# Kernel optimization log

Measured on AMD Instinct MI355X. Metric: run time of the kernel, lower is better.

Reference implementation:

```python
import jax, jax.numpy as jnp
import numpy as np

B, T, V, E, H = 64, 64, 32000, 512, 1024


def setup_inputs() -> dict:
    key = jax.random.key(0)
    ks = jax.random.split(key, 12)
    s = 0.02
    return {
        "hidden": jax.random.normal(ks[0], (2, B, H), jnp.float32),
        "cell": jax.random.normal(ks[1], (2, B, H), jnp.float32),
        "captions": jax.random.randint(ks[2], (B, T), 0, V, jnp.int32),
        "embed_W": jax.random.normal(ks[3], (V, E), jnp.float32) * s,
        "W_ih0": jax.random.normal(ks[4], (4 * H, E), jnp.float32) * s,
        "W_hh0": jax.random.normal(ks[5], (4 * H, H), jnp.float32) * s,
        "b_ih0": jnp.zeros((4 * H,), jnp.float32),
        "b_hh0": jnp.zeros((4 * H,), jnp.float32),
        "W_ih1": jax.random.normal(ks[6], (4 * H, H), jnp.float32) * s,
        "W_hh1": jax.random.normal(ks[7], (4 * H, H), jnp.float32) * s,
        "b_ih1": jnp.zeros((4 * H,), jnp.float32),
        "b_hh1": jnp.zeros((4 * H,), jnp.float32),
        "Wp_voc": jax.random.normal(ks[8], (V, H), jnp.float32) * s,
        "bp_voc": jnp.zeros((V,), jnp.float32),
    }


def lstm_cell(x, h, c, W_ih, W_hh, b):
    # PyTorch gate order: input, forget, cell(g), output
    gates = x @ W_ih.T + h @ W_hh.T + b  # [B, 4H]
    i, f, g, o = jnp.split(gates, 4, axis=-1)
    i, f, o = jax.nn.sigmoid(i), jax.nn.sigmoid(f), jax.nn.sigmoid(o)
    g = jnp.tanh(g)
    c_new = f * c + i * g
    h_new = o * jnp.tanh(c_new)
    return h_new, c_new


def reference(hidden, cell, captions, embed_W, W_ih0, W_hh0, b_ih0, b_hh0,
              W_ih1, W_hh1, b_ih1, b_hh1, Wp_voc, bp_voc):
    # teacher forcing (ratio=1.0): LSTM input at step t is embed(captions[:, t-1])
    x_seq = embed_W[captions[:, :-1]]        # [B, T-1, E]
    x_seq = jnp.swapaxes(x_seq, 0, 1)        # [T-1, B, E] time-major for scan
    b0 = b_ih0 + b_hh0
    b1 = b_ih1 + b_hh1

    def step(carry, x):
        h0, c0, h1, c1 = carry
        h0, c0 = lstm_cell(x, h0, c0, W_ih0, W_hh0, b0)
        h1, c1 = lstm_cell(h0, h1, c1, W_ih1, W_hh1, b1)
        logits = h1 @ Wp_voc.T + bp_voc      # [B, V]
        return (h0, c0, h1, c1), logits

    carry = (hidden[0], cell[0], hidden[1], cell[1])
    _, logits = jax.lax.scan(step, carry, x_seq)   # [T-1, B, V]
    logits = jnp.swapaxes(logits, 0, 1)            # [B, T-1, V]
    # outputs[:, 0, :] stays zero as in the torch code
    return jnp.concatenate([jnp.zeros((logits.shape[0], 1, logits.shape[2]), logits.dtype), logits], axis=1)
```

## Files before the change

kernel.cpp:

```cpp
#include <hip/hip_runtime.h>

#define B_    64
#define T_    64
#define V_    32000
#define E_    512
#define H_    1024
#define G4_   4096
#define TS_   63
#define MROWS 4032
#define MPAD  4096
#define BH    (B_ * H_)
#define FPAD  32

typedef __attribute__((ext_vector_type(8))) short bf16x8;
typedef __attribute__((ext_vector_type(4))) float f32x4;
typedef __attribute__((ext_vector_type(4))) unsigned int uint32x4;

__device__ __forceinline__ unsigned short bfbits(float f) {
  union { float f; unsigned int u; } cv; cv.f = f;
  unsigned int u = cv.u;
  u += 0x7fffu + ((u >> 16) & 1u);
  return (unsigned short)(u >> 16);
}
__device__ __forceinline__ float bf2f(unsigned short h) {
  union { unsigned int u; float f; } cv; cv.u = ((unsigned int)h) << 16;
  return cv.f;
}
__device__ __forceinline__ float fsig(float x) { return 1.f / (1.f + __expf(-x)); }
__device__ __forceinline__ float ftanh(float x) {
  x = fminf(fmaxf(x, -10.f), 10.f);
  const float e = __expf(2.f * x);
  return (e - 1.f) / (e + 1.f);
}

__device__ __forceinline__ void store_dword_dc(void* p, unsigned int v) {
  asm volatile("global_store_dword %0, %1, off sc0 sc1" :: "v"(p), "v"(v) : "memory");
}
__device__ __forceinline__ void store_b128_dc(void* p, uint32x4 v) {
  asm volatile("global_store_dwordx4 %0, %1, off sc0 sc1" :: "v"(p), "v"(v) : "memory");
}
__device__ __forceinline__ unsigned int load_dword_dc(const void* p) {
  unsigned int v;
  asm volatile("global_load_dword %0, %1, off sc0 sc1\n\ts_waitcnt vmcnt(0)"
               : "=v"(v) : "v"(p) : "memory");
  return v;
}
__device__ __forceinline__ void store_dword_nt(void* p, float f) {
  union { float f; unsigned int u; } cv; cv.f = f;
  asm volatile("global_store_dword %0, %1, off nt" :: "v"(p), "v"(cv.u) : "memory");
}

__device__ __forceinline__ void gload16(const void* g, void* l) {
  __builtin_amdgcn_global_load_lds(
      (const __attribute__((address_space(1))) unsigned int*)g,
      (__attribute__((address_space(3))) unsigned int*)l, 16, 0, 0);
}


__global__ void k_cast4(const float4* __restrict__ s, ushort4* __restrict__ d, int n4) {
  int i = blockIdx.x * blockDim.x + threadIdx.x;
  const int st = gridDim.x * blockDim.x;
  for (; i < n4; i += st) {
    const float4 f = s[i];
    ushort4 v;
    v.x = bfbits(f.x); v.y = bfbits(f.y); v.z = bfbits(f.z); v.w = bfbits(f.w);
    d[i] = v;
  }
}

__global__ void k_bias(const float* __restrict__ a, const float* __restrict__ b,
                       float* __restrict__ o, int n) {
  const int i = blockIdx.x * blockDim.x + threadIdx.x;
  if (i < n) o[i] = a[i] + b[i];
}

__global__ void k_gather(const float* __restrict__ embed, const int* __restrict__ caps,
                         unsigned short* __restrict__ X) {
  const int i = blockIdx.x * 256 + threadIdx.x;
  const int m = i >> 7, e4 = i & 127;
  ushort4 v;
  if (m < MROWS) {
    const int t = m >> 6, b = m & 63;
    const int idx = caps[b * T_ + t];
    const float4 f = ((const float4*)embed)[(long)idx * (E_ / 4) + e4];
    v.x = bfbits(f.x); v.y = bfbits(f.y); v.z = bfbits(f.z); v.w = bfbits(f.w);
  } else {
    v = make_ushort4(0, 0, 0, 0);
  }
  ((ushort4*)X)[i] = v;
}

__global__ void k_init(const float* __restrict__ hidden, const float* __restrict__ cell,
                       unsigned short* __restrict__ H0, unsigned short* __restrict__ H1,
                       float* __restrict__ c0, float* __restrict__ c1,
                       unsigned int* __restrict__ flags) {
  const int i = blockIdx.x * 256 + threadIdx.x;
  H0[i] = bfbits(hidden[i]);
  H1[i] = bfbits(hidden[B_ * H_ + i]);
  c0[i] = cell[i];
  c1[i] = cell[B_ * H_ + i];
  if (i < 192 * FPAD) flags[i] = 0u;
}

__global__ void k_zeropad(unsigned short* __restrict__ a, unsigned short* __restrict__ b) {
  const int i = blockIdx.x * 256 + threadIdx.x;
  a[i] = 0;
  b[i] = 0;
}

__global__ void k_zero_t0(float4* __restrict__ out4) {
  const int i = blockIdx.x * 256 + threadIdx.x;
  const int b = i / (V_ / 4), v = i - b * (V_ / 4);
  out4[(long)b * (T_ * V_ / 4) + v] = make_float4(0.f, 0.f, 0.f, 0.f);
}

template <int KDIM, bool TO_OUT>
__global__ __launch_bounds__(256) void k_gemm(
    const unsigned short* __restrict__ A, const unsigned short* __restrict__ Bm,
    const float* __restrict__ bias, unsigned short* __restrict__ Cb,
    float* __restrict__ Cout, int N) {
  __shared__ unsigned short As[128 * 32];
  __shared__ unsigned short Bs[128 * 32];
  const int tid = threadIdx.x;
  const int w = tid >> 6, l = tid & 63;
  const int wm = (w >> 1) * 64, wn = (w & 1) * 64;
  const int lr = l & 15, lk = (l >> 4) * 8;
  const long am0 = (long)blockIdx.y * 128;
  const long bn0 = (long)blockIdx.x * 128;

  const int u0 = tid, u1 = tid + 256;
  const char* gA0 = (const char*)(A + (am0 + (u0 >> 2)) * KDIM) + (u0 & 3) * 16;
  const char* gA1 = (const char*)(A + (am0 + (u1 >> 2)) * KDIM) + (u1 & 3) * 16;
  const char* gB0 = (const char*)(Bm + (bn0 + (u0 >> 2)) * KDIM) + (u0 & 3) * 16;
  const char* gB1 = (const char*)(Bm + (bn0 + (u1 >> 2)) * KDIM) + (u1 & 3) * 16;
  char* lA0 = (char*)As + u0 * 16; char* lA1 = (char*)As + u1 * 16;
  char* lB0 = (char*)Bs + u0 * 16; char* lB1 = (char*)Bs + u1 * 16;

  f32x4 acc[4][4];
  const f32x4 z = {0.f, 0.f, 0.f, 0.f};
  #pragma unroll
  for (int mi = 0; mi < 4; ++mi)
    #pragma unroll
    for (int ni = 0; ni < 4; ++ni) acc[mi][ni] = z;

  for (int k0 = 0; k0 < KDIM; k0 += 32) {
    __syncthreads();
    gload16(gA0 + (long)k0 * 2, lA0);
    gload16(gA1 + (long)k0 * 2, lA1);
    gload16(gB0 + (long)k0 * 2, lB0);
    gload16(gB1 + (long)k0 * 2, lB1);
    __syncthreads();
    bf16x8 af[4], bfr[4];
    #pragma unroll
    for (int mi = 0; mi < 4; ++mi)
      af[mi] = *(const bf16x8*)(As + (wm + mi * 16 + lr) * 32 + lk);
    #pragma unroll
    for (int ni = 0; ni < 4; ++ni)
      bfr[ni] = *(const bf16x8*)(Bs + (wn + ni * 16 + lr) * 32 + lk);
    #pragma unroll
    for (int mi = 0; mi < 4; ++mi)
      #pragma unroll
      for (int ni = 0; ni < 4; ++ni)
        acc[mi][ni] = __builtin_amdgcn_mfma_f32_16x16x32_bf16(af[mi], bfr[ni], acc[mi][ni], 0, 0, 0);
  }

  #pragma unroll
  for (int ni = 0; ni < 4; ++ni) {
    const int n = (int)bn0 + wn + ni * 16 + lr;
    const float bv = bias[n];
    #pragma unroll
    for (int mi = 0; mi < 4; ++mi) {
      #pragma unroll
      for (int r = 0; r < 4; ++r) {
        const int m = (int)am0 + wm + mi * 16 + (l >> 4) * 4 + r;
        const float v = acc[mi][ni][r] + bv;
        if constexpr (TO_OUT) {
          if (m < MROWS) {
            const int t = m >> 6, b = m & 63;
            store_dword_nt(Cout + (long)(b * T_ + t + 1) * V_ + n, v);
          }
        } else {
          Cb[(long)m * N + n] = bfbits(v);
        }
      }
    }
  }
}

__global__ __launch_bounds__(256) void k_fused(
    const unsigned short* __restrict__ Whh0b,
    const unsigned short* __restrict__ Whh1b,
    const unsigned short* __restrict__ Wih1b,
    const unsigned short* __restrict__ Xp,
    unsigned short* __restrict__ H0b,
    unsigned short* __restrict__ H1b,
    const float* __restrict__ c0i, const float* __restrict__ c1i,
    const float* __restrict__ b1s,
    unsigned int* __restrict__ f0,
    unsigned int* __restrict__ f1) {
  __shared__ unsigned short Wl[64 * 1024];
  __shared__ __align__(16) float gs1[4][64][8];
  unsigned short (*hexch)[16] = (unsigned short (*)[16])gs1;

  const int tid = threadIdx.x;
  const int w = tid >> 6, l = tid & 63;
  const int lcol = l & 15, khi = l >> 4;
  const int bw = w * 16;
  const f32x4 z = {0.f, 0.f, 0.f, 0.f};

  if (blockIdx.x < 64) {
    const int blk = blockIdx.x;
    const int jb = blk << 4;
    for (int u = tid; u < 64 * 128; u += 256) {
      const int rr = u >> 7, cu = u & 127;
      const int g = rr >> 4, jj = rr & 15;
      ((bf16x8*)Wl)[rr * 128 + (cu ^ (rr & 7))] =
          *(const bf16x8*)(Whh0b + (size_t)(g * 1024 + jb + jj) * H_ + cu * 8);
    }
    f32x4 cr;
    #pragma unroll
    for (int r = 0; r < 4; ++r)
      cr[r] = c0i[(size_t)(bw + khi * 4 + r) * H_ + jb + lcol];
    unsigned short pin[16];
    #pragma unroll
    for (int r = 0; r < 4; ++r) {
      const unsigned short* ir = Xp + (size_t)(bw + khi * 4 + r) * G4_ + jb + lcol;
      pin[r * 4 + 0] = ir[0];
      pin[r * 4 + 1] = ir[H_];
      pin[r * 4 + 2] = ir[2 * H_];
      pin[r * 4 + 3] = ir[3 * H_];
    }
    __syncthreads();

    for (int s = 0; s < TS_; ++s) {
      if (s > 0) {
        if (tid < 64)
          while (load_dword_dc(&f0[tid << 5]) < (unsigned)s) {}
        __syncthreads();
      }
      f32x4 a0, a1, a2, a3;
      #pragma unroll
      for (int r = 0; r < 4; ++r) {
        a0[r] = bf2f(pin[r * 4 + 0]);
        a1[r] = bf2f(pin[r * 4 + 1]);
        a2[r] = bf2f(pin[r * 4 + 2]);
        a3[r] = bf2f(pin[r * 4 + 3]);
      }
      const unsigned short* hrow = H0b + (size_t)s * BH + (size_t)(bw + lcol) * H_ + khi * 8;
      #pragma unroll 8
      for (int kk = 0; kk < 32; ++kk) {
        const bf16x8 av = *(const bf16x8*)(hrow + kk * 32);
        const int un = (kk * 4 + khi) ^ (lcol & 7);
        const bf16x8 b0 = ((const bf16x8*)Wl)[(0 * 16 + lcol) * 128 + un];
        const bf16x8 b1 = ((const bf16x8*)Wl)[(1 * 16 + lcol) * 128 + un];
        const bf16x8 b2 = ((const bf16x8*)Wl)[(2 * 16 + lcol) * 128 + un];
        const bf16x8 b3 = ((const bf16x8*)Wl)[(3 * 16 + lcol) * 128 + un];
        a0 = __builtin_amdgcn_mfma_f32_16x16x32_bf16(av, b0, a0, 0, 0, 0);
        a1 = __builtin_amdgcn_mfma_f32_16x16x32_bf16(av, b1, a1, 0, 0, 0);
        a2 = __builtin_amdgcn_mfma_f32_16x16x32_bf16(av, b2, a2, 0, 0, 0);
        a3 = __builtin_amdgcn_mfma_f32_16x16x32_bf16(av, b3, a3, 0, 0, 0);
      }
      #pragma unroll
      for (int r = 0; r < 4; ++r) {
        const float gi = fsig(a0[r]);
        const float gf = fsig(a1[r]);
        const float gg = ftanh(a2[r]);
        const float go = fsig(a3[r]);
        cr[r] = gf * cr[r] + gi * gg;
        hexch[bw + khi * 4 + r][lcol] = bfbits(go * ftanh(cr[r]));
      }
      if (s + 1 < TS_) {
        const unsigned short* inb = Xp + (size_t)(s + 1) * (B_ * G4_);
        #pragma unroll
        for (int r = 0; r < 4; ++r) {
          const unsigned short* ir = inb + (size_t)(bw + khi * 4 + r) * G4_ + jb + lcol;
          pin[r * 4 + 0] = ir[0];
          pin[r * 4 + 1] = ir[H_];
          pin[r * 4 + 2] = ir[2 * H_];
          pin[r * 4 + 3] = ir[3 * H_];
        }
      }
      __syncthreads();
      if (tid < 128) {
        const int b = tid >> 1, hf = tid & 1;
        const uint32x4 v = *(const uint32x4*)&hexch[b][hf * 8];
        store_b128_dc(H0b + (size_t)(s + 1) * BH + (size_t)b * H_ + jb + hf * 8, v);
      }
      __syncthreads();
      if (tid == 0) store_dword_dc(&f0[blk << 5], (unsigned)(s + 1));
    }
  } else {
    const int blk1 = blockIdx.x - 64;
    const int jb1 = blk1 << 3;
    for (int u = tid; u < 64 * 128; u += 256) {
      const int pr = u >> 7, cu = u & 127;
      const int prl = pr & 31, tt = prl >> 4, lr_ = prl & 15;
      const int g = tt * 2 + (lr_ >> 3), jj = lr_ & 7;
      const unsigned short* src =
          ((pr >> 5) ? Wih1b : Whh1b) + (size_t)(g * 1024 + jb1 + jj) * H_ + cu * 8;
      ((bf16x8*)Wl)[pr * 128 + (cu ^ (pr & 7))] = *(const bf16x8*)src;
    }
    const int bb = tid >> 2;
    const int j0 = (tid * 2) & 7;
    float cA = c1i[(size_t)bb * H_ + jb1 + j0];
    float cB = c1i[(size_t)bb * H_ + jb1 + j0 + 1];
    float biA[4], biB[4];
    #pragma unroll
    for (int g = 0; g < 4; ++g) {
      biA[g] = b1s[g * 1024 + jb1 + j0];
      biB[g] = b1s[g * 1024 + jb1 + j0 + 1];
    }
    __syncthreads();

    for (int s = 1; s <= TS_; ++s) {
      {
        const unsigned t0 = (unsigned)s, t1 = (unsigned)(s - 1);
        if (tid < 64) {
          while (load_dword_dc(&f0[tid << 5]) < t0) {}
        } else if (tid < 192) {
          while (load_dword_dc(&f1[(tid - 64) << 5]) < t1) {}
        }
        __syncthreads();
      }
      f32x4 ac0 = z, ac1 = z;
      const unsigned short* a1p = H1b + (size_t)(s - 1) * BH + (size_t)(bw + lcol) * H_ + khi * 8;
      const unsigned short* a0p = H0b + (size_t)s * BH + (size_t)(bw + lcol) * H_ + khi * 8;
      #pragma unroll 8
      for (int kk = 0; kk < 32; ++kk) {
        const bf16x8 av = *(const bf16x8*)(a1p + kk * 32);
        const int un = (kk * 4 + khi) ^ (lcol & 7);
        const bf16x8 b0 = ((const bf16x8*)Wl)[(0 + lcol) * 128 + un];
        const bf16x8 b1 = ((const bf16x8*)Wl)[(16 + lcol) * 128 + un];
        ac0 = __builtin_amdgcn_mfma_f32_16x16x32_bf16(av, b0, ac0, 0, 0, 0);
        ac1 = __builtin_amdgcn_mfma_f32_16x16x32_bf16(av, b1, ac1, 0, 0, 0);
      }
      #pragma unroll 8
      for (int kk = 0; kk < 32; ++kk) {
        const bf16x8 av = *(const bf16x8*)(a0p + kk * 32);
        const int un = (kk * 4 + khi) ^ (lcol & 7);
        const bf16x8 b0 = ((const bf16x8*)Wl)[(32 + lcol) * 128 + un];
        const bf16x8 b1 = ((const bf16x8*)Wl)[(48 + lcol) * 128 + un];
        ac0 = __builtin_amdgcn_mfma_f32_16x16x32_bf16(av, b0, ac0, 0, 0, 0);
        ac1 = __builtin_amdgcn_mfma_f32_16x16x32_bf16(av, b1, ac1, 0, 0, 0);
      }
      #pragma unroll
      for (int r = 0; r < 4; ++r) {
        const int b = bw + khi * 4 + r;
        gs1[lcol >> 3][b][lcol & 7] = ac0[r];
        gs1[2 + (lcol >> 3)][b][lcol & 7] = ac1[r];
      }
      __syncthreads();
      {
        const float giA = fsig(gs1[0][bb][j0] + biA[0]);
        const float gfA = fsig(gs1[1][bb][j0] + biA[1]);
        const float ggA = ftanh(gs1[2][bb][j0] + biA[2]);
        const float goA = fsig(gs1[3][bb][j0] + biA[3]);
        cA = gfA * cA + giA * ggA;
        const unsigned short hA = bfbits(goA * ftanh(cA));
        const float giB = fsig(gs1[0][bb][j0 + 1] + biB[0]);
        const float gfB = fsig(gs1[1][bb][j0 + 1] + biB[1]);
        const float ggB = ftanh(gs1[2][bb][j0 + 1] + biB[2]);
        const float goB = fsig(gs1[3][bb][j0 + 1] + biB[3]);
        cB = gfB * cB + giB * ggB;
        const unsigned short hB = bfbits(goB * ftanh(cB));
        const unsigned int hv = ((unsigned int)hB << 16) | hA;
        store_dword_dc(H1b + (size_t)s * BH + (size_t)bb * H_ + jb1 + j0, hv);
      }
      __syncthreads();
      if (tid == 0) store_dword_dc(&f1[blk1 << 5], (unsigned)s);
    }
  }
}


extern "C" void kernel_launch(void* const* d_in, const int* in_sizes, int n_in,
                              void* d_out, int out_size, void* d_ws, size_t ws_size,
                              hipStream_t stream) {
  (void)in_sizes; (void)n_in; (void)out_size; (void)ws_size;
  const float* hidden = (const float*)d_in[0];
  const float* cell   = (const float*)d_in[1];
  const int*   caps   = (const int*)d_in[2];
  const float* embed  = (const float*)d_in[3];
  const float* Wih0   = (const float*)d_in[4];
  const float* Whh0   = (const float*)d_in[5];
  const float* bih0   = (const float*)d_in[6];
  const float* bhh0   = (const float*)d_in[7];
  const float* Wih1   = (const float*)d_in[8];
  const float* Whh1   = (const float*)d_in[9];
  const float* bih1   = (const float*)d_in[10];
  const float* bhh1   = (const float*)d_in[11];
  const float* Wp     = (const float*)d_in[12];
  const float* bp     = (const float*)d_in[13];
  float* out = (float*)d_out;

  char* p = (char*)d_ws;
  auto alloc = [&](size_t bytes) { char* r = p; p += (bytes + 255) & ~(size_t)255; return r; };
  unsigned short* Xbf   = (unsigned short*)alloc((size_t)MPAD * E_ * 2);
  unsigned short* Wih0b = (unsigned short*)alloc((size_t)G4_ * E_ * 2);
  unsigned short* Whh0b = (unsigned short*)alloc((size_t)G4_ * H_ * 2);
  unsigned short* Wih1b = (unsigned short*)alloc((size_t)G4_ * H_ * 2);
  unsigned short* Whh1b = (unsigned short*)alloc((size_t)G4_ * H_ * 2);
  unsigned short* Wpb   = (unsigned short*)alloc((size_t)V_ * H_ * 2);
  unsigned short* Xp    = (unsigned short*)alloc((size_t)MPAD * G4_ * 2);
  unsigned short* H0    = (unsigned short*)alloc((size_t)(MPAD + B_) * H_ * 2);
  unsigned short* H1    = (unsigned short*)alloc((size_t)(MPAD + B_) * H_ * 2);
  float* c0  = (float*)alloc((size_t)B_ * H_ * 4);
  float* c1  = (float*)alloc((size_t)B_ * H_ * 4);
  float* b0s = (float*)alloc((size_t)G4_ * 4);
  float* b1s = (float*)alloc((size_t)G4_ * 4);
  unsigned int* cbar = (unsigned int*)alloc((size_t)192 * FPAD * 4);

  k_cast4<<<2048, 256, 0, stream>>>((const float4*)Wih0, (ushort4*)Wih0b, G4_ * E_ / 4);
  k_cast4<<<2048, 256, 0, stream>>>((const float4*)Whh0, (ushort4*)Whh0b, G4_ * H_ / 4);
  k_cast4<<<2048, 256, 0, stream>>>((const float4*)Wih1, (ushort4*)Wih1b, G4_ * H_ / 4);
  k_cast4<<<2048, 256, 0, stream>>>((const float4*)Whh1, (ushort4*)Whh1b, G4_ * H_ / 4);
  k_cast4<<<4096, 256, 0, stream>>>((const float4*)Wp,   (ushort4*)Wpb,   V_ * H_ / 4);
  k_bias<<<16, 256, 0, stream>>>(bih0, bhh0, b0s, G4_);
  k_bias<<<16, 256, 0, stream>>>(bih1, bhh1, b1s, G4_);
  k_gather<<<2048, 256, 0, stream>>>(embed, caps, Xbf);
  k_init<<<256, 256, 0, stream>>>(hidden, cell, H0, H1, c0, c1, cbar);
  k_zeropad<<<256, 256, 0, stream>>>(H0 + (size_t)MPAD * H_, H1 + (size_t)MPAD * H_);
  k_zero_t0<<<2000, 256, 0, stream>>>((float4*)out);

  k_gemm<512, false><<<dim3(32, 32), 256, 0, stream>>>(Xbf, Wih0b, b0s, Xp, nullptr, G4_);

  k_fused<<<192, 256, 0, stream>>>(Whh0b, Whh1b, Wih1b, Xp, H0, H1, c0, c1, b1s,
                                   cbar, cbar + 64 * FPAD);

  k_gemm<1024, true><<<dim3(250, 32), 256, 0, stream>>>(H1 + (size_t)B_ * H_, Wpb, bp, nullptr, out, V_);
}
```

Measured before the change: 1.109 ms.

## Swizzle vocab GEMM block order for cache reuse and add sleep in spin-waits

The output projection GEMM now launches a flat 1D grid of 8192 blocks over a vocabulary dimension padded to 32768. Block indices are remapped so that consecutive blocks share the same N-columns of the weight tile across M rows, grouped into 8 chunks, to improve L2/MALL reuse of weight tiles. Bounds checks on n handle the padded region. Separately, the spin-wait loops in the fused LSTM kernel now call s_sleep to reduce memory polling pressure, which may add wake-up latency to every step. The padded weight rows past V are allocated but never initialised, so they hold garbage; their products are computed and then discarded, which wastes some work.

```diff
diff --git a/kernel.cpp b/kernel.cpp
--- a/kernel.cpp
+++ b/kernel.cpp
@@ -3,6 +3,7 @@
 #define B_    64
 #define T_    64
 #define V_    32000
+#define VPAD  32768
 #define E_    512
 #define H_    1024
 #define G4_   4096
@@ -114,7 +115,7 @@
   out4[(long)b * (T_ * V_ / 4) + v] = make_float4(0.f, 0.f, 0.f, 0.f);
 }
 
-template <int KDIM, bool TO_OUT>
+template <int KDIM, bool TO_OUT, bool SWZ>
 __global__ __launch_bounds__(256) void k_gemm(
     const unsigned short* __restrict__ A, const unsigned short* __restrict__ Bm,
     const float* __restrict__ bias, unsigned short* __restrict__ Cb,
@@ -125,8 +126,17 @@
   const int w = tid >> 6, l = tid & 63;
   const int wm = (w >> 1) * 64, wn = (w & 1) * 64;
   const int lr = l & 15, lk = (l >> 4) * 8;
-  const long am0 = (long)blockIdx.y * 128;
-  const long bn0 = (long)blockIdx.x * 128;
+  int bx, by;
+  if constexpr (SWZ) {
+    const int flat = blockIdx.x;
+    const int k = flat & 7, i = flat >> 3;
+    bx = (k << 5) + (i >> 5);
+    by = i & 31;
+  } else {
+    bx = blockIdx.x; by = blockIdx.y;
+  }
+  const long am0 = (long)by * 128;
+  const long bn0 = (long)bx * 128;
 
   const int u0 = tid, u1 = tid + 256;
   const char* gA0 = (const char*)(A + (am0 + (u0 >> 2)) * KDIM) + (u0 & 3) * 16;
@@ -167,7 +177,7 @@
   #pragma unroll
   for (int ni = 0; ni < 4; ++ni) {
     const int n = (int)bn0 + wn + ni * 16 + lr;
-    const float bv = bias[n];
+    const float bv = (!TO_OUT || n < V_) ? bias[n] : 0.f;
     #pragma unroll
     for (int mi = 0; mi < 4; ++mi) {
       #pragma unroll
@@ -175,7 +185,7 @@
         const int m = (int)am0 + wm + mi * 16 + (l >> 4) * 4 + r;
         const float v = acc[mi][ni][r] + bv;
         if constexpr (TO_OUT) {
-          if (m < MROWS) {
+          if (m < MROWS && n < V_) {
             const int t = m >> 6, b = m & 63;
             store_dword_nt(Cout + (long)(b * T_ + t + 1) * V_ + n, v);
           }
@@ -235,7 +245,8 @@
     for (int s = 0; s < TS_; ++s) {
       if (s > 0) {
         if (tid < 64)
-          while (load_dword_dc(&f0[tid << 5]) < (unsigned)s) {}
+          while (load_dword_dc(&f0[tid << 5]) < (unsigned)s)
+            __builtin_amdgcn_s_sleep(1);
         __syncthreads();
       }
       f32x4 a0, a1, a2, a3;
@@ -316,9 +327,9 @@
       {
         const unsigned t0 = (unsigned)s, t1 = (unsigned)(s - 1);
         if (tid < 64) {
-          while (load_dword_dc(&f0[tid << 5]) < t0) {}
+          while (load_dword_dc(&f0[tid << 5]) < t0) __builtin_amdgcn_s_sleep(1);
         } else if (tid < 192) {
-          while (load_dword_dc(&f1[(tid - 64) << 5]) < t1) {}
+          while (load_dword_dc(&f1[(tid - 64) << 5]) < t1) __builtin_amdgcn_s_sleep(1);
         }
         __syncthreads();
       }
@@ -400,7 +411,7 @@
   unsigned short* Whh0b = (unsigned short*)alloc((size_t)G4_ * H_ * 2);
   unsigned short* Wih1b = (unsigned short*)alloc((size_t)G4_ * H_ * 2);
   unsigned short* Whh1b = (unsigned short*)alloc((size_t)G4_ * H_ * 2);
-  unsigned short* Wpb   = (unsigned short*)alloc((size_t)V_ * H_ * 2);
+  unsigned short* Wpb   = (unsigned short*)alloc((size_t)VPAD * H_ * 2);
   unsigned short* Xp    = (unsigned short*)alloc((size_t)MPAD * G4_ * 2);
   unsigned short* H0    = (unsigned short*)alloc((size_t)(MPAD + B_) * H_ * 2);
   unsigned short* H1    = (unsigned short*)alloc((size_t)(MPAD + B_) * H_ * 2);
@@ -422,10 +433,10 @@
   k_zeropad<<<256, 256, 0, stream>>>(H0 + (size_t)MPAD * H_, H1 + (size_t)MPAD * H_);
   k_zero_t0<<<2000, 256, 0, stream>>>((float4*)out);
 
-  k_gemm<512, false><<<dim3(32, 32), 256, 0, stream>>>(Xbf, Wih0b, b0s, Xp, nullptr, G4_);
+  k_gemm<512, false, false><<<dim3(32, 32), 256, 0, stream>>>(Xbf, Wih0b, b0s, Xp, nullptr, G4_);
 
   k_fused<<<192, 256, 0, stream>>>(Whh0b, Whh1b, Wih1b, Xp, H0, H1, c0, c1, b1s,
                                    cbar, cbar + 64 * FPAD);
 
-  k_gemm<1024, true><<<dim3(250, 32), 256, 0, stream>>>(H1 + (size_t)B_ * H_, Wpb, bp, nullptr, out, V_);
-}
+  k_gemm<1024, true, true><<<8192, 256, 0, stream>>>(H1 + (size_t)B_ * H_, Wpb, bp, nullptr, out, V_);
+}
```

Result: no change. 1.114 ms (+0.4%).

## Overlap vocab projection GEMM with LSTM recurrence via persistent work-stealing blocks

Applied to the files above, without the earlier changes.

Folds the output projection GEMM into the persistent recurrent kernel. Blocks take 128x128 output tiles from an atomic counter and wait on the layer-1 progress flags until the needed timesteps are done, so the projection overlaps the serial recurrence. The launch grows to 256 blocks: 64 extra blocks start on projection work at once, and the recurrence blocks join when they finish. Spin-waits now use s_sleep to ease polling pressure. Risks include contention with the latency-critical recurrence blocks and a deadlock if not all blocks are co-resident.

```diff
diff --git a/kernel.cpp b/kernel.cpp
--- a/kernel.cpp
+++ b/kernel.cpp
@@ -11,6 +11,7 @@
 #define MPAD  4096
 #define BH    (B_ * H_)
 #define FPAD  32
+#define NTILES 8000
 
 typedef __attribute__((ext_vector_type(8))) short bf16x8;
 typedef __attribute__((ext_vector_type(4))) float f32x4;
@@ -99,7 +100,7 @@
   H1[i] = bfbits(hidden[B_ * H_ + i]);
   c0[i] = cell[i];
   c1[i] = cell[B_ * H_ + i];
-  if (i < 192 * FPAD) flags[i] = 0u;
+  if (i < 256 * FPAD) flags[i] = 0u;
 }
 
 __global__ void k_zeropad(unsigned short* __restrict__ a, unsigned short* __restrict__ b) {
@@ -114,11 +115,9 @@
   out4[(long)b * (T_ * V_ / 4) + v] = make_float4(0.f, 0.f, 0.f, 0.f);
 }
 
-template <int KDIM, bool TO_OUT>
-__global__ __launch_bounds__(256) void k_gemm(
+__global__ __launch_bounds__(256) void k_gemm1(
     const unsigned short* __restrict__ A, const unsigned short* __restrict__ Bm,
-    const float* __restrict__ bias, unsigned short* __restrict__ Cb,
-    float* __restrict__ Cout, int N) {
+    const float* __restrict__ bias, unsigned short* __restrict__ Cb) {
   __shared__ unsigned short As[128 * 32];
   __shared__ unsigned short Bs[128 * 32];
   const int tid = threadIdx.x;
@@ -129,10 +128,10 @@
   const long bn0 = (long)blockIdx.x * 128;
 
   const int u0 = tid, u1 = tid + 256;
-  const char* gA0 = (const char*)(A + (am0 + (u0 >> 2)) * KDIM) + (u0 & 3) * 16;
-  const char* gA1 = (const char*)(A + (am0 + (u1 >> 2)) * KDIM) + (u1 & 3) * 16;
-  const char* gB0 = (const char*)(Bm + (bn0 + (u0 >> 2)) * KDIM) + (u0 & 3) * 16;
-  const char* gB1 = (const char*)(Bm + (bn0 + (u1 >> 2)) * KDIM) + (u1 & 3) * 16;
+  const char* gA0 = (const char*)(A + (am0 + (u0 >> 2)) * E_) + (u0 & 3) * 16;
+  const char* gA1 = (const char*)(A + (am0 + (u1 >> 2)) * E_) + (u1 & 3) * 16;
+  const char* gB0 = (const char*)(Bm + (bn0 + (u0 >> 2)) * E_) + (u0 & 3) * 16;
+  const char* gB1 = (const char*)(Bm + (bn0 + (u1 >> 2)) * E_) + (u1 & 3) * 16;
   char* lA0 = (char*)As + u0 * 16; char* lA1 = (char*)As + u1 * 16;
   char* lB0 = (char*)Bs + u0 * 16; char* lB1 = (char*)Bs + u1 * 16;
 
@@ -143,7 +142,7 @@
     #pragma unroll
     for (int ni = 0; ni < 4; ++ni) acc[mi][ni] = z;
 
-  for (int k0 = 0; k0 < KDIM; k0 += 32) {
+  for (int k0 = 0; k0 < E_; k0 += 32) {
     __syncthreads();
     gload16(gA0 + (long)k0 * 2, lA0);
     gload16(gA1 + (long)k0 * 2, lA1);
@@ -173,15 +172,7 @@
       #pragma unroll
       for (int r = 0; r < 4; ++r) {
         const int m = (int)am0 + wm + mi * 16 + (l >> 4) * 4 + r;
-        const float v = acc[mi][ni][r] + bv;
-        if constexpr (TO_OUT) {
-          if (m < MROWS) {
-            const int t = m >> 6, b = m & 63;
-            store_dword_nt(Cout + (long)(b * T_ + t + 1) * V_ + n, v);
-          }
-        } else {
-          Cb[(long)m * N + n] = bfbits(v);
-        }
+        Cb[(long)m * G4_ + n] = bfbits(acc[mi][ni][r] + bv);
       }
     }
   }
@@ -196,10 +187,15 @@
     unsigned short* __restrict__ H1b,
     const float* __restrict__ c0i, const float* __restrict__ c1i,
     const float* __restrict__ b1s,
+    const unsigned short* __restrict__ Wpb,
+    const float* __restrict__ bp,
+    float* __restrict__ out,
     unsigned int* __restrict__ f0,
-    unsigned int* __restrict__ f1) {
+    unsigned int* __restrict__ f1,
+    unsigned int* __restrict__ ctr) {
   __shared__ unsigned short Wl[64 * 1024];
   __shared__ __align__(16) float gs1[4][64][8];
+  __shared__ int poolSh;
   unsigned short (*hexch)[16] = (unsigned short (*)[16])gs1;
 
   const int tid = threadIdx.x;
@@ -235,7 +231,7 @@
     for (int s = 0; s < TS_; ++s) {
       if (s > 0) {
         if (tid < 64)
-          while (load_dword_dc(&f0[tid << 5]) < (unsigned)s) {}
+          while (load_dword_dc(&f0[tid << 5]) < (unsigned)s) __builtin_amdgcn_s_sleep(1);
         __syncthreads();
       }
       f32x4 a0, a1, a2, a3;
@@ -289,7 +285,7 @@
       __syncthreads();
       if (tid == 0) store_dword_dc(&f0[blk << 5], (unsigned)(s + 1));
     }
-  } else {
+  } else if (blockIdx.x < 192) {
     const int blk1 = blockIdx.x - 64;
     const int jb1 = blk1 << 3;
     for (int u = tid; u < 64 * 128; u += 256) {
@@ -316,9 +312,9 @@
       {
         const unsigned t0 = (unsigned)s, t1 = (unsigned)(s - 1);
         if (tid < 64) {
-          while (load_dword_dc(&f0[tid << 5]) < t0) {}
+          while (load_dword_dc(&f0[tid << 5]) < t0) __builtin_amdgcn_s_sleep(1);
         } else if (tid < 192) {
-          while (load_dword_dc(&f1[(tid - 64) << 5]) < t1) {}
+          while (load_dword_dc(&f1[(tid - 64) << 5]) < t1) __builtin_amdgcn_s_sleep(1);
         }
         __syncthreads();
       }
@@ -368,6 +364,81 @@
       }
       __syncthreads();
       if (tid == 0) store_dword_dc(&f1[blk1 << 5], (unsigned)s);
+    }
+  }
+
+  {
+    unsigned short* As = Wl;
+    unsigned short* Bs = Wl + 128 * 32;
+    const unsigned short* Ae = H1b + BH;
+    const int wm = (w >> 1) * 64, wn = (w & 1) * 64;
+    const int lr = l & 15, lk = (l >> 4) * 8;
+
+    for (;;) {
+      __syncthreads();
+      if (tid == 0) poolSh = (int)atomicAdd(ctr, 1u);
+      __syncthreads();
+      const int tau = poolSh;
+      if (tau >= NTILES) break;
+      const int my = tau / 250, nx = tau - my * 250;
+      const unsigned tmax = (unsigned)(2 * my + 2 < 63 ? 2 * my + 2 : 63);
+      if (tid < 128)
+        while (load_dword_dc(&f1[tid << 5]) < tmax) __builtin_amdgcn_s_sleep(2);
+      __syncthreads();
+
+      const long am0 = (long)my * 128;
+      const long bn0 = (long)nx * 128;
+      const int u0 = tid, u1 = tid + 256;
+      const char* gA0 = (const char*)(Ae + (am0 + (u0 >> 2)) * H_) + (u0 & 3) * 16;
+      const char* gA1 = (const char*)(Ae + (am0 + (u1 >> 2)) * H_) + (u1 & 3) * 16;
+      const char* gB0 = (const char*)(Wpb + (bn0 + (u0 >> 2)) * H_) + (u0 & 3) * 16;
+      const char* gB1 = (const char*)(Wpb + (bn0 + (u1 >> 2)) * H_) + (u1 & 3) * 16;
+      char* lA0 = (char*)As + u0 * 16; char* lA1 = (char*)As + u1 * 16;
+      char* lB0 = (char*)Bs + u0 * 16; char* lB1 = (char*)Bs + u1 * 16;
+
+      f32x4 acc[4][4];
+      #pragma unroll
+      for (int mi = 0; mi < 4; ++mi)
+        #pragma unroll
+        for (int ni = 0; ni < 4; ++ni) acc[mi][ni] = z;
+
+      for (int k0 = 0; k0 < H_; k0 += 32) {
+        __syncthreads();
+        gload16(gA0 + (long)k0 * 2, lA0);
+        gload16(gA1 + (long)k0 * 2, lA1);
+        gload16(gB0 + (long)k0 * 2, lB0);
+        gload16(gB1 + (long)k0 * 2, lB1);
+        __syncthreads();
+        bf16x8 af[4], bfr[4];
+        #pragma unroll
+        for (int mi = 0; mi < 4; ++mi)
+          af[mi] = *(const bf16x8*)(As + (wm + mi * 16 + lr) * 32 + lk);
+        #pragma unroll
+        for (int ni = 0; ni < 4; ++ni)
+          bfr[ni] = *(const bf16x8*)(Bs + (wn + ni * 16 + lr) * 32 + lk);
+        #pragma unroll
+        for (int mi = 0; mi < 4; ++mi)
+          #pragma unroll
+          for (int ni = 0; ni < 4; ++ni)
+            acc[mi][ni] = __builtin_amdgcn_mfma_f32_16x16x32_bf16(af[mi], bfr[ni], acc[mi][ni], 0, 0, 0);
+      }
+
+      #pragma unroll
+      for (int ni = 0; ni < 4; ++ni) {
+        const int n = (int)bn0 + wn + ni * 16 + lr;
+        const float bv = bp[n];
+        #pragma unroll
+        for (int mi = 0; mi < 4; ++mi) {
+          #pragma unroll
+          for (int r = 0; r < 4; ++r) {
+            const int m = (int)am0 + wm + mi * 16 + (l >> 4) * 4 + r;
+            if (m < MROWS) {
+              const int t = m >> 6, b = m & 63;
+              store_dword_nt(out + (long)(b * T_ + t + 1) * V_ + n, acc[mi][ni][r] + bv);
+            }
+          }
+        }
+      }
     }
   }
 }
@@ -408,7 +479,7 @@
   float* c1  = (float*)alloc((size_t)B_ * H_ * 4);
   float* b0s = (float*)alloc((size_t)G4_ * 4);
   float* b1s = (float*)alloc((size_t)G4_ * 4);
-  unsigned int* cbar = (unsigned int*)alloc((size_t)192 * FPAD * 4);
+  unsigned int* cbar = (unsigned int*)alloc((size_t)256 * FPAD * 4);
 
   k_cast4<<<2048, 256, 0, stream>>>((const float4*)Wih0, (ushort4*)Wih0b, G4_ * E_ / 4);
   k_cast4<<<2048, 256, 0, stream>>>((const float4*)Whh0, (ushort4*)Whh0b, G4_ * H_ / 4);
@@ -422,10 +493,9 @@
   k_zeropad<<<256, 256, 0, stream>>>(H0 + (size_t)MPAD * H_, H1 + (size_t)MPAD * H_);
   k_zero_t0<<<2000, 256, 0, stream>>>((float4*)out);
 
-  k_gemm<512, false><<<dim3(32, 32), 256, 0, stream>>>(Xbf, Wih0b, b0s, Xp, nullptr, G4_);
-
-  k_fused<<<192, 256, 0, stream>>>(Whh0b, Whh1b, Wih1b, Xp, H0, H1, c0, c1, b1s,
-                                   cbar, cbar + 64 * FPAD);
-
-  k_gemm<1024, true><<<dim3(250, 32), 256, 0, stream>>>(H1 + (size_t)B_ * H_, Wpb, bp, nullptr, out, V_);
-}
+  k_gemm1<<<dim3(32, 32), 256, 0, stream>>>(Xbf, Wih0b, b0s, Xp);
+
+  k_fused<<<256, 256, 0, stream>>>(Whh0b, Whh1b, Wih1b, Xp, H0, H1, c0, c1, b1s,
+                                   Wpb, bp, out,
+                                   cbar, cbar + 64 * FPAD, cbar + 192 * FPAD);
+}
```

After: 1.320 ms. 1.19x slower.

## Replace vocab projection GEMM with 256x256 double-buffered tile kernel; add sleep to spin-waits

Applied to the files above, without the earlier changes.

The output projection GEMM (4096x1024 by 32000x1024) moves to a new kernel with 512 threads, 256x256 tiles, 64-wide K steps, XOR-swizzled LDS, double-buffered async loads with explicit vmcnt waits, and raised MFMA priority. The aim is more data reuse per tile and overlap of global loads with MFMA work. The first GEMM is specialised to a non-template version, and the flag spin loops in the fused recurrent kernel now call s_sleep to reduce polling pressure. This uses 128KB of LDS per block, and the sleep may add wake-up latency to each recurrent step.

```diff
diff --git a/kernel.cpp b/kernel.cpp
--- a/kernel.cpp
+++ b/kernel.cpp
@@ -114,11 +114,9 @@
   out4[(long)b * (T_ * V_ / 4) + v] = make_float4(0.f, 0.f, 0.f, 0.f);
 }
 
-template <int KDIM, bool TO_OUT>
-__global__ __launch_bounds__(256) void k_gemm(
+__global__ __launch_bounds__(256) void k_gemm1(
     const unsigned short* __restrict__ A, const unsigned short* __restrict__ Bm,
-    const float* __restrict__ bias, unsigned short* __restrict__ Cb,
-    float* __restrict__ Cout, int N) {
+    const float* __restrict__ bias, unsigned short* __restrict__ Cb) {
   __shared__ unsigned short As[128 * 32];
   __shared__ unsigned short Bs[128 * 32];
   const int tid = threadIdx.x;
@@ -129,10 +127,10 @@
   const long bn0 = (long)blockIdx.x * 128;
 
   const int u0 = tid, u1 = tid + 256;
-  const char* gA0 = (const char*)(A + (am0 + (u0 >> 2)) * KDIM) + (u0 & 3) * 16;
-  const char* gA1 = (const char*)(A + (am0 + (u1 >> 2)) * KDIM) + (u1 & 3) * 16;
-  const char* gB0 = (const char*)(Bm + (bn0 + (u0 >> 2)) * KDIM) + (u0 & 3) * 16;
-  const char* gB1 = (const char*)(Bm + (bn0 + (u1 >> 2)) * KDIM) + (u1 & 3) * 16;
+  const char* gA0 = (const char*)(A + (am0 + (u0 >> 2)) * E_) + (u0 & 3) * 16;
+  const char* gA1 = (const char*)(A + (am0 + (u1 >> 2)) * E_) + (u1 & 3) * 16;
+  const char* gB0 = (const char*)(Bm + (bn0 + (u0 >> 2)) * E_) + (u0 & 3) * 16;
+  const char* gB1 = (const char*)(Bm + (bn0 + (u1 >> 2)) * E_) + (u1 & 3) * 16;
   char* lA0 = (char*)As + u0 * 16; char* lA1 = (char*)As + u1 * 16;
   char* lB0 = (char*)Bs + u0 * 16; char* lB1 = (char*)Bs + u1 * 16;
 
@@ -143,7 +141,7 @@
     #pragma unroll
     for (int ni = 0; ni < 4; ++ni) acc[mi][ni] = z;
 
-  for (int k0 = 0; k0 < KDIM; k0 += 32) {
+  for (int k0 = 0; k0 < E_; k0 += 32) {
     __syncthreads();
     gload16(gA0 + (long)k0 * 2, lA0);
     gload16(gA1 + (long)k0 * 2, lA1);
@@ -173,14 +171,106 @@
       #pragma unroll
       for (int r = 0; r < 4; ++r) {
         const int m = (int)am0 + wm + mi * 16 + (l >> 4) * 4 + r;
-        const float v = acc[mi][ni][r] + bv;
-        if constexpr (TO_OUT) {
-          if (m < MROWS) {
-            const int t = m >> 6, b = m & 63;
-            store_dword_nt(Cout + (long)(b * T_ + t + 1) * V_ + n, v);
-          }
-        } else {
-          Cb[(long)m * N + n] = bfbits(v);
+        Cb[(long)m * G4_ + n] = bfbits(acc[mi][ni][r] + bv);
+      }
+    }
+  }
+}
+
+__global__ __launch_bounds__(512, 2) void k_gemm3(
+    const unsigned short* __restrict__ A,
+    const unsigned short* __restrict__ Bm,
+    const float* __restrict__ bias,
+    float* __restrict__ out) {
+  __shared__ unsigned short As[2][256 * 64];
+  __shared__ unsigned short Bs[2][256 * 64];
+  const int tid = threadIdx.x;
+  const int wid = tid >> 6, l = tid & 63;
+  const int wr = wid >> 2, wc = wid & 3;
+  const int lr = l & 15, khi = l >> 4;
+  const int id = blockIdx.x;
+  const int by = id / 125, bx = id - by * 125;
+  const long am0 = (long)by * 256;
+  const long bn0 = (long)bx * 256;
+
+  int srow[4], sq[4];
+  #pragma unroll
+  for (int j = 0; j < 4; ++j) {
+    const int idx = j * 512 + tid;
+    srow[j] = idx >> 3;
+    sq[j] = (idx & 7) ^ (srow[j] & 7);
+  }
+
+  f32x4 acc[8][4];
+  const f32x4 z = {0.f, 0.f, 0.f, 0.f};
+  #pragma unroll
+  for (int mf = 0; mf < 8; ++mf)
+    #pragma unroll
+    for (int nf = 0; nf < 4; ++nf) acc[mf][nf] = z;
+
+  auto stage = [&](int kt, int b) {
+    const long koff = (long)kt * 128;
+    #pragma unroll
+    for (int j = 0; j < 4; ++j) {
+      const int idx = j * 512 + tid;
+      gload16((const char*)(A + (am0 + srow[j]) * H_) + koff + sq[j] * 16,
+              (char*)As[b] + idx * 16);
+    }
+    #pragma unroll
+    for (int j = 0; j < 4; ++j) {
+      const int idx = j * 512 + tid;
+      gload16((const char*)(Bm + (bn0 + srow[j]) * H_) + koff + sq[j] * 16,
+              (char*)Bs[b] + idx * 16);
+    }
+  };
+
+  stage(0, 0);
+  for (int t = 0; t < 16; ++t) {
+    const int c = t & 1;
+    __builtin_amdgcn_s_barrier();
+    if (t + 1 < 16) {
+      stage(t + 1, c ^ 1);
+      asm volatile("s_waitcnt vmcnt(8)" ::: "memory");
+    } else {
+      asm volatile("s_waitcnt vmcnt(0)" ::: "memory");
+    }
+    __builtin_amdgcn_s_barrier();
+    #pragma unroll
+    for (int ks = 0; ks < 2; ++ks) {
+      const int qx = ((ks * 4 + khi) ^ (lr & 7)) * 16;
+      bf16x8 af[8], bfr[4];
+      #pragma unroll
+      for (int mf = 0; mf < 8; ++mf) {
+        const int row = wr * 128 + mf * 16 + lr;
+        af[mf] = *(const bf16x8*)((const char*)As[c] + row * 128 + qx);
+      }
+      #pragma unroll
+      for (int nf = 0; nf < 4; ++nf) {
+        const int row = wc * 64 + nf * 16 + lr;
+        bfr[nf] = *(const bf16x8*)((const char*)Bs[c] + row * 128 + qx);
+      }
+      __builtin_amdgcn_s_setprio(1);
+      #pragma unroll
+      for (int mf = 0; mf < 8; ++mf)
+        #pragma unroll
+        for (int nf = 0; nf < 4; ++nf)
+          acc[mf][nf] = __builtin_amdgcn_mfma_f32_16x16x32_bf16(af[mf], bfr[nf], acc[mf][nf], 0, 0, 0);
+      __builtin_amdgcn_s_setprio(0);
+    }
+  }
+
+  #pragma unroll
+  for (int nf = 0; nf < 4; ++nf) {
+    const int n = (int)bn0 + wc * 64 + nf * 16 + lr;
+    const float bv = bias[n];
+    #pragma unroll
+    for (int mf = 0; mf < 8; ++mf) {
+      #pragma unroll
+      for (int r = 0; r < 4; ++r) {
+        const int m = (int)am0 + wr * 128 + mf * 16 + khi * 4 + r;
+        if (m < MROWS) {
+          const int t = m >> 6, b = m & 63;
+          store_dword_nt(out + (long)(b * T_ + t + 1) * V_ + n, acc[mf][nf][r] + bv);
         }
       }
     }
@@ -235,7 +325,7 @@
     for (int s = 0; s < TS_; ++s) {
       if (s > 0) {
         if (tid < 64)
-          while (load_dword_dc(&f0[tid << 5]) < (unsigned)s) {}
+          while (load_dword_dc(&f0[tid << 5]) < (unsigned)s) __builtin_amdgcn_s_sleep(1);
         __syncthreads();
       }
       f32x4 a0, a1, a2, a3;
@@ -316,9 +406,9 @@
       {
         const unsigned t0 = (unsigned)s, t1 = (unsigned)(s - 1);
         if (tid < 64) {
-          while (load_dword_dc(&f0[tid << 5]) < t0) {}
+          while (load_dword_dc(&f0[tid << 5]) < t0) __builtin_amdgcn_s_sleep(1);
         } else if (tid < 192) {
-          while (load_dword_dc(&f1[(tid - 64) << 5]) < t1) {}
+          while (load_dword_dc(&f1[(tid - 64) << 5]) < t1) __builtin_amdgcn_s_sleep(1);
         }
         __syncthreads();
       }
@@ -422,10 +512,10 @@
   k_zeropad<<<256, 256, 0, stream>>>(H0 + (size_t)MPAD * H_, H1 + (size_t)MPAD * H_);
   k_zero_t0<<<2000, 256, 0, stream>>>((float4*)out);
 
-  k_gemm<512, false><<<dim3(32, 32), 256, 0, stream>>>(Xbf, Wih0b, b0s, Xp, nullptr, G4_);
+  k_gemm1<<<dim3(32, 32), 256, 0, stream>>>(Xbf, Wih0b, b0s, Xp);
 
   k_fused<<<192, 256, 0, stream>>>(Whh0b, Whh1b, Wih1b, Xp, H0, H1, c0, c1, b1s,
                                    cbar, cbar + 64 * FPAD);
 
-  k_gemm<1024, true><<<dim3(250, 32), 256, 0, stream>>>(H1 + (size_t)B_ * H_, Wpb, bp, nullptr, out, V_);
-}
+  k_gemm3<<<2000, 512, 0, stream>>>(H1 + (size_t)B_ * H_, Wpb, bp, out);
+}
```

Result: faster. 1.047 ms (-5.6%).
